# Optimization experiments

Hardware: AMD Instinct MI355X
Metric: run time of the kernel (lower is better)

The kernel has to match this reference:

```python
import jax, jax.numpy as jnp
import numpy as np

B, R, C, OUT, IN = 64, 2048, 32, 32, 16
ROUTING_ITERS = 3


def squash(s, axis=-1):
    s_norm = jnp.linalg.norm(s, axis=axis, keepdims=True)
    scale = s_norm ** 2 / (1.0 + s_norm ** 2)
    return scale * s / (s_norm + 1e-8)


def setup_inputs() -> dict:
    key = jax.random.key(0)
    k1, k2 = jax.random.split(key)
    x = jax.random.normal(k1, (B, R, IN), dtype=jnp.float32)
    W = jax.random.normal(k2, (1, R, C, OUT, IN), dtype=jnp.float32)
    return {"x": x, "W": W}


def reference(x, W):
    # u_hat[b,r,c,o] = sum_i W[r,c,o,i] * x[b,r,i]
    u_hat = jnp.einsum('rcoi,bri->brco', W[0], x)  # [B,R,C,OUT]
    b = jnp.zeros((x.shape[0], R, C), dtype=x.dtype)
    v = None
    for i in range(ROUTING_ITERS):
        c = jax.nn.softmax(b, axis=2)[..., None]       # [B,R,C,1]
        s = jnp.sum(c * u_hat, axis=1)                 # [B,C,OUT]
        v = squash(s)                                  # [B,C,OUT]
        if i < ROUTING_ITERS - 1:
            b = b + jnp.einsum('brco,bco->brc', u_hat, v)
    return v
```

## Files before the change

### kernel.cpp

```cpp
#include <hip/hip_runtime.h>


#define Bn 64
#define Rn 2048
#define Cn 32
#define On 32
#define In 16
#define RCH 16
#define NRC2 (Rn / RCH)
#define NG 2

typedef _Float16 half4v __attribute__((ext_vector_type(4)));
typedef float floatx4 __attribute__((ext_vector_type(4)));

__global__ __launch_bounds__(256)
void wconv(const float* __restrict__ W, _Float16* __restrict__ Wh) {
    const size_t i = ((size_t)blockIdx.x * 256 + threadIdx.x) * 8;
    const float4 a = *(const float4*)(W + i);
    const float4 b = *(const float4*)(W + i + 4);
    union { _Float16 h[8]; uint4 u; } pk;
    pk.h[0] = (_Float16)a.x; pk.h[1] = (_Float16)a.y;
    pk.h[2] = (_Float16)a.z; pk.h[3] = (_Float16)a.w;
    pk.h[4] = (_Float16)b.x; pk.h[5] = (_Float16)b.y;
    pk.h[6] = (_Float16)b.z; pk.h[7] = (_Float16)b.w;
    *(uint4*)(Wh + i) = pk.u;
}

template <int PHASE>
__global__ __launch_bounds__(512, 2)
void upass(const float* __restrict__ x, const _Float16* __restrict__ Wh,
           const float* __restrict__ vroute, float* __restrict__ s_part) {
    const int tid  = threadIdx.x;
    const int w    = tid >> 6;
    const int lane = tid & 63;
    const int q    = lane >> 4;
    const int bl   = lane & 15;

    const int L  = blockIdx.x;
    const int bg = (L >> 3) & 1;
    const int rc = (L & 7) | ((L >> 4) << 3);
    const int b0 = bg * 32;

    __shared__ __attribute__((aligned(16))) _Float16 xs[RCH * 32 * 20];
    __shared__ __attribute__((aligned(16))) float sums[2][2][16][8];

    floatx4 v00[4], v01[4], v10[4], v11[4];
    if constexpr (PHASE > 0) {
        const float* vb0 = vroute + (size_t)(b0 + bl) * 1024 + 4 * q;
        const float* vb1 = vroute + (size_t)(b0 + 16 + bl) * 1024 + 4 * q;
#pragma unroll
        for (int t = 0; t < 4; ++t) {
            const int co = (w * 4 + t) * 32;
            v00[t] = *(const floatx4*)(vb0 + co);
            v01[t] = *(const floatx4*)(vb0 + co + 16);
            v10[t] = *(const floatx4*)(vb1 + co);
            v11[t] = *(const floatx4*)(vb1 + co + 16);
        }
    }

#pragma unroll
    for (int k = 0; k < 4; ++k) {
        const int u  = tid + k * 512;
        const int rr = u >> 7, bb = (u >> 2) & 31, iq = u & 3;
        const float4 xv = *(const float4*)(x + (size_t)(b0 + bb) * (Rn * In) +
                                           (size_t)(rc * RCH + rr) * In + iq * 4);
        union { _Float16 h[4]; uint2 u2; } p;
        p.h[0] = (_Float16)xv.x; p.h[1] = (_Float16)xv.y;
        p.h[2] = (_Float16)xv.z; p.h[3] = (_Float16)xv.w;
        *(uint2*)(xs + (rr * 32 + bb) * 20 + iq * 4) = p.u2;
    }
    __syncthreads();

    floatx4 accS0[8], accS1[8];
#pragma unroll
    for (int m = 0; m < 8; ++m) {
        accS0[m] = (floatx4){0.f, 0.f, 0.f, 0.f};
        accS1[m] = (floatx4){0.f, 0.f, 0.f, 0.f};
    }

    const _Float16* Wp = Wh + ((size_t)(rc * RCH) * 1024 + w * 128 + bl) * 16 + 4 * q;

    half4v a[8];
#pragma unroll
    for (int m = 0; m < 8; ++m) a[m] = *(const half4v*)(Wp + m * 256);
    half4v bf0 = *(const half4v*)(xs + bl * 20 + 4 * q);
    half4v bf1 = *(const half4v*)(xs + (16 + bl) * 20 + 4 * q);

    for (int rr = 0; rr < RCH; ++rr) {
        const int rn = (rr + 1 < RCH) ? rr + 1 : rr;
        const _Float16* Wn = Wp + (size_t)rn * 16384;

        if constexpr (PHASE == 0) {
#pragma unroll
            for (int m = 0; m < 8; ++m) {
                accS0[m] = __builtin_amdgcn_mfma_f32_16x16x16f16(a[m], bf0, accS0[m], 0, 0, 0);
                accS1[m] = __builtin_amdgcn_mfma_f32_16x16x16f16(a[m], bf1, accS1[m], 0, 0, 0);
            }
            const half4v bn0 = *(const half4v*)(xs + (rn * 32 + bl) * 20 + 4 * q);
            const half4v bn1 = *(const half4v*)(xs + (rn * 32 + 16 + bl) * 20 + 4 * q);
#pragma unroll
            for (int m = 0; m < 8; ++m) a[m] = *(const half4v*)(Wn + m * 256);
            bf0 = bn0; bf1 = bn1;
        } else {
            floatx4 D0[8], D1[8];
#pragma unroll
            for (int m = 0; m < 8; ++m) {
                D0[m] = __builtin_amdgcn_mfma_f32_16x16x16f16(
                            a[m], bf0, (floatx4){0.f, 0.f, 0.f, 0.f}, 0, 0, 0);
                D1[m] = __builtin_amdgcn_mfma_f32_16x16x16f16(
                            a[m], bf1, (floatx4){0.f, 0.f, 0.f, 0.f}, 0, 0, 0);
            }

            const half4v bn0 = *(const half4v*)(xs + (rn * 32 + bl) * 20 + 4 * q);
            const half4v bn1 = *(const half4v*)(xs + (rn * 32 + 16 + bl) * 20 + 4 * q);
#pragma unroll
            for (int m = 0; m < 8; ++m) a[m] = *(const half4v*)(Wn + m * 256);
            bf0 = bn0; bf1 = bn1;

            float e0[4], e1[4], se0 = 0.f, se1 = 0.f;
#pragma unroll
            for (int t = 0; t < 4; ++t) {
                float lp0 = D0[2*t].x * v00[t].x + D0[2*t].y * v00[t].y +
                            D0[2*t].z * v00[t].z + D0[2*t].w * v00[t].w +
                            D0[2*t+1].x * v01[t].x + D0[2*t+1].y * v01[t].y +
                            D0[2*t+1].z * v01[t].z + D0[2*t+1].w * v01[t].w;
                float lp1 = D1[2*t].x * v10[t].x + D1[2*t].y * v10[t].y +
                            D1[2*t].z * v10[t].z + D1[2*t].w * v10[t].w +
                            D1[2*t+1].x * v11[t].x + D1[2*t+1].y * v11[t].y +
                            D1[2*t+1].z * v11[t].z + D1[2*t+1].w * v11[t].w;
                lp0 += __shfl_xor(lp0, 16, 64);
                lp0 += __shfl_xor(lp0, 32, 64);
                lp1 += __shfl_xor(lp1, 16, 64);
                lp1 += __shfl_xor(lp1, 32, 64);
                e0[t] = __expf(lp0); se0 += e0[t];
                e1[t] = __expf(lp1); se1 += e1[t];
            }
            if (lane < 32) sums[rr & 1][q][bl][w] = (q == 0) ? se0 : se1;
            asm volatile("s_waitcnt lgkmcnt(0)" ::: "memory");
            __builtin_amdgcn_s_barrier();
            asm volatile("" ::: "memory");
            const floatx4 sa0 = *(const floatx4*)(&sums[rr & 1][0][bl][0]);
            const floatx4 sa1 = *(const floatx4*)(&sums[rr & 1][0][bl][4]);
            const floatx4 sb0 = *(const floatx4*)(&sums[rr & 1][1][bl][0]);
            const floatx4 sb1 = *(const floatx4*)(&sums[rr & 1][1][bl][4]);
            const float tot0 = sa0.x + sa0.y + sa0.z + sa0.w +
                               sa1.x + sa1.y + sa1.z + sa1.w;
            const float tot1 = sb0.x + sb0.y + sb0.z + sb0.w +
                               sb1.x + sb1.y + sb1.z + sb1.w;
            const float winv0 = __builtin_amdgcn_rcpf(tot0);
            const float winv1 = __builtin_amdgcn_rcpf(tot1);
#pragma unroll
            for (int t = 0; t < 4; ++t) {
                const float wt0 = e0[t] * winv0;
                const float wt1 = e1[t] * winv1;
                accS0[2*t]   += wt0 * D0[2*t];
                accS0[2*t+1] += wt0 * D0[2*t+1];
                accS1[2*t]   += wt1 * D1[2*t];
                accS1[2*t+1] += wt1 * D1[2*t+1];
            }
        }
    }

    const size_t sb = (((size_t)rc * 64 + b0 + bl)) * 1024 + w * 128 + 4 * q;
#pragma unroll
    for (int m = 0; m < 8; ++m) {
        *(floatx4*)(s_part + sb + m * 16) = accS0[m];
        *(floatx4*)(s_part + sb + (size_t)16 * 1024 + m * 16) = accS1[m];
    }
}

__global__ __launch_bounds__(256)
void reduce_squash(const float* __restrict__ sp, float scale,
                   float* __restrict__ vout, const float* __restrict__ vprev,
                   float* __restrict__ vsum) {
    const int b = blockIdx.x >> 3, oct = blockIdx.x & 7;
    const int t = threadIdx.x;
    const int kg = t >> 5, ci = t & 31;
    const size_t base = (size_t)b * 1024 + (size_t)oct * 128 + (size_t)ci * 4;

    floatx4 acc0 = (floatx4){0.f, 0.f, 0.f, 0.f};
    floatx4 acc1 = (floatx4){0.f, 0.f, 0.f, 0.f};
#pragma unroll
    for (int k = kg * 16; k < kg * 16 + 16; k += 2) {
        acc0 += *(const floatx4*)(sp + (size_t)k * 65536 + base);
        acc1 += *(const floatx4*)(sp + (size_t)(k + 1) * 65536 + base);
    }
    const floatx4 acc = acc0 + acc1;

    __shared__ __attribute__((aligned(16))) float red[8][128];
    *(floatx4*)(&red[kg][ci * 4]) = acc;
    __syncthreads();

    if (t < 128) {
        float s = 0.f;
#pragma unroll
        for (int g = 0; g < 8; ++g) s += red[g][t];
        s *= scale;
        float n2 = s * s;
        n2 += __shfl_xor(n2, 1, 64);
        n2 += __shfl_xor(n2, 2, 64);
        n2 += __shfl_xor(n2, 4, 64);
        n2 += __shfl_xor(n2, 8, 64);
        n2 += __shfl_xor(n2, 16, 64);
        const float norm = sqrtf(n2);
        const float f = (n2 / (1.f + n2)) / (norm + 1e-8f);
        const float vv = s * f;
        const size_t o = (size_t)b * 1024 + (size_t)oct * 128 + t;
        if (vout) vout[o] = vv;
        if (vsum) vsum[o] = vv + vprev[o];
    }
}

extern "C" void kernel_launch(void* const* d_in, const int* in_sizes, int n_in,
                              void* d_out, int out_size, void* d_ws, size_t ws_size,
                              hipStream_t stream) {
    const float* x = (const float*)d_in[0];
    const float* W = (const float*)d_in[1];
    float* out = (float*)d_out;

    char* ws = (char*)d_ws;
    _Float16* Wh  = (_Float16*)ws;
    float* s_part = (float*)(ws + (size_t)67108864);
    float* v1     = (float*)(ws + (size_t)67108864 + 33554432);
    float* v12    = (float*)(ws + (size_t)67108864 + 33554432 + 262144);

    const int ublocks = NG * NRC2;

    wconv<<<16384, 256, 0, stream>>>(W, Wh);

    upass<0><<<ublocks, 512, 0, stream>>>(x, Wh, nullptr, s_part);
    reduce_squash<<<512, 256, 0, stream>>>(s_part, 1.f / 32.f, v1, nullptr, nullptr);

    upass<1><<<ublocks, 512, 0, stream>>>(x, Wh, v1, s_part);
    reduce_squash<<<512, 256, 0, stream>>>(s_part, 1.f, nullptr, v1, v12);

    upass<2><<<ublocks, 512, 0, stream>>>(x, Wh, v12, s_part);
    reduce_squash<<<512, 256, 0, stream>>>(s_part, 1.f, out, nullptr, nullptr);
}
```

Before: 297.5 us.

## Fuse routing passes into one cooperative kernel with grid syncs

Replaces the six separate upass and reduce_squash launches with a single cooperative kernel of 256 blocks that uses grid-wide syncs between phases. The x tile is converted to fp16 and staged in shared memory once and reused across all three routing iterations instead of being reloaded each pass. This removes kernel launch gaps and repeated x loads, at the cost of grid barrier overhead and a residency requirement that all blocks fit at once.

```diff
diff --git a/kernel.cpp b/kernel.cpp
--- a/kernel.cpp
+++ b/kernel.cpp
@@ -1,4 +1,5 @@
 #include <hip/hip_runtime.h>
+#include <hip/hip_cooperative_groups.h>
 
 
 #define Bn 64
@@ -9,6 +10,8 @@
 #define RCH 16
 #define NRC2 (Rn / RCH)
 #define NG 2
+
+namespace cg = cooperative_groups;
 
 typedef _Float16 half4v __attribute__((ext_vector_type(4)));
 typedef float floatx4 __attribute__((ext_vector_type(4)));
@@ -27,22 +30,10 @@
 }
 
 template <int PHASE>
-__global__ __launch_bounds__(512, 2)
-void upass(const float* __restrict__ x, const _Float16* __restrict__ Wh,
-           const float* __restrict__ vroute, float* __restrict__ s_part) {
-    const int tid  = threadIdx.x;
-    const int w    = tid >> 6;
-    const int lane = tid & 63;
-    const int q    = lane >> 4;
-    const int bl   = lane & 15;
-
-    const int L  = blockIdx.x;
-    const int bg = (L >> 3) & 1;
-    const int rc = (L & 7) | ((L >> 4) << 3);
-    const int b0 = bg * 32;
-
-    __shared__ __attribute__((aligned(16))) _Float16 xs[RCH * 32 * 20];
-    __shared__ __attribute__((aligned(16))) float sums[2][2][16][8];
+__device__ __forceinline__ void upass_dev(
+    const _Float16* __restrict__ Wh, const float* __restrict__ vroute,
+    float* __restrict__ s_part, const _Float16* xs, float (&sums)[2][2][16][8],
+    int w, int lane, int q, int bl, int rc, int b0) {
 
     floatx4 v00[4], v01[4], v10[4], v11[4];
     if constexpr (PHASE > 0) {
@@ -57,19 +48,6 @@
             v11[t] = *(const floatx4*)(vb1 + co + 16);
         }
     }
-
-#pragma unroll
-    for (int k = 0; k < 4; ++k) {
-        const int u  = tid + k * 512;
-        const int rr = u >> 7, bb = (u >> 2) & 31, iq = u & 3;
-        const float4 xv = *(const float4*)(x + (size_t)(b0 + bb) * (Rn * In) +
-                                           (size_t)(rc * RCH + rr) * In + iq * 4);
-        union { _Float16 h[4]; uint2 u2; } p;
-        p.h[0] = (_Float16)xv.x; p.h[1] = (_Float16)xv.y;
-        p.h[2] = (_Float16)xv.z; p.h[3] = (_Float16)xv.w;
-        *(uint2*)(xs + (rr * 32 + bb) * 20 + iq * 4) = p.u2;
-    }
-    __syncthreads();
 
     floatx4 accS0[8], accS1[8];
 #pragma unroll
@@ -169,12 +147,14 @@
     }
 }
 
-__global__ __launch_bounds__(256)
-void reduce_squash(const float* __restrict__ sp, float scale,
-                   float* __restrict__ vout, const float* __restrict__ vprev,
-                   float* __restrict__ vsum) {
-    const int b = blockIdx.x >> 3, oct = blockIdx.x & 7;
-    const int t = threadIdx.x;
+__device__ __forceinline__ void rs_dev(
+    const float* __restrict__ sp, float scale,
+    float* __restrict__ vout, const float* __restrict__ vprev,
+    float* __restrict__ vsum, float (&red)[2][8][128], int tid, int bx) {
+    const int vb = bx * 2 + (tid >> 8);
+    const int half = tid >> 8;
+    const int b = vb >> 3, oct = vb & 7;
+    const int t = tid & 255;
     const int kg = t >> 5, ci = t & 31;
     const size_t base = (size_t)b * 1024 + (size_t)oct * 128 + (size_t)ci * 4;
 
@@ -187,14 +167,13 @@
     }
     const floatx4 acc = acc0 + acc1;
 
-    __shared__ __attribute__((aligned(16))) float red[8][128];
-    *(floatx4*)(&red[kg][ci * 4]) = acc;
+    *(floatx4*)(&red[half][kg][ci * 4]) = acc;
     __syncthreads();
 
     if (t < 128) {
         float s = 0.f;
 #pragma unroll
-        for (int g = 0; g < 8; ++g) s += red[g][t];
+        for (int g = 0; g < 8; ++g) s += red[half][g][t];
         s *= scale;
         float n2 = s * s;
         n2 += __shfl_xor(n2, 1, 64);
@@ -211,6 +190,55 @@
     }
 }
 
+__global__ __launch_bounds__(512, 2)
+void mega(const float* __restrict__ x, const _Float16* __restrict__ Wh,
+          float* __restrict__ s_part, float* __restrict__ v1,
+          float* __restrict__ v12, float* __restrict__ out) {
+    const int tid  = threadIdx.x;
+    const int w    = tid >> 6;
+    const int lane = tid & 63;
+    const int q    = lane >> 4;
+    const int bl   = lane & 15;
+
+    const int L  = blockIdx.x;
+    const int bg = (L >> 3) & 1;
+    const int rc = (L & 7) | ((L >> 4) << 3);
+    const int b0 = bg * 32;
+
+    __shared__ __attribute__((aligned(16))) _Float16 xs[RCH * 32 * 20];
+    __shared__ __attribute__((aligned(16))) float sums[2][2][16][8];
+    __shared__ __attribute__((aligned(16))) float red[2][8][128];
+
+#pragma unroll
+    for (int k = 0; k < 4; ++k) {
+        const int u  = tid + k * 512;
+        const int rr = u >> 7, bb = (u >> 2) & 31, iq = u & 3;
+        const float4 xv = *(const float4*)(x + (size_t)(b0 + bb) * (Rn * In) +
+                                           (size_t)(rc * RCH + rr) * In + iq * 4);
+        union { _Float16 h[4]; uint2 u2; } p;
+        p.h[0] = (_Float16)xv.x; p.h[1] = (_Float16)xv.y;
+        p.h[2] = (_Float16)xv.z; p.h[3] = (_Float16)xv.w;
+        *(uint2*)(xs + (rr * 32 + bb) * 20 + iq * 4) = p.u2;
+    }
+    __syncthreads();
+
+    cg::grid_group gg = cg::this_grid();
+
+    upass_dev<0>(Wh, nullptr, s_part, xs, sums, w, lane, q, bl, rc, b0);
+    __threadfence(); gg.sync();
+    rs_dev(s_part, 1.f / 32.f, v1, nullptr, nullptr, red, tid, L);
+    __threadfence(); gg.sync();
+
+    upass_dev<1>(Wh, v1, s_part, xs, sums, w, lane, q, bl, rc, b0);
+    __threadfence(); gg.sync();
+    rs_dev(s_part, 1.f, nullptr, v1, v12, red, tid, L);
+    __threadfence(); gg.sync();
+
+    upass_dev<2>(Wh, v12, s_part, xs, sums, w, lane, q, bl, rc, b0);
+    __threadfence(); gg.sync();
+    rs_dev(s_part, 1.f, out, nullptr, nullptr, red, tid, L);
+}
+
 extern "C" void kernel_launch(void* const* d_in, const int* in_sizes, int n_in,
                               void* d_out, int out_size, void* d_ws, size_t ws_size,
                               hipStream_t stream) {
@@ -224,16 +252,10 @@
     float* v1     = (float*)(ws + (size_t)67108864 + 33554432);
     float* v12    = (float*)(ws + (size_t)67108864 + 33554432 + 262144);
 
-    const int ublocks = NG * NRC2;
-
     wconv<<<16384, 256, 0, stream>>>(W, Wh);
 
-    upass<0><<<ublocks, 512, 0, stream>>>(x, Wh, nullptr, s_part);
-    reduce_squash<<<512, 256, 0, stream>>>(s_part, 1.f / 32.f, v1, nullptr, nullptr);
-
-    upass<1><<<ublocks, 512, 0, stream>>>(x, Wh, v1, s_part);
-    reduce_squash<<<512, 256, 0, stream>>>(s_part, 1.f, nullptr, v1, v12);
-
-    upass<2><<<ublocks, 512, 0, stream>>>(x, Wh, v12, s_part);
-    reduce_squash<<<512, 256, 0, stream>>>(s_part, 1.f, out, nullptr, nullptr);
-}
+    void* args[6] = {(void*)&x, (void*)&Wh, (void*)&s_part,
+                     (void*)&v1, (void*)&v12, (void*)&out};
+    hipLaunchCooperativeKernel((const void*)mega, dim3(NG * NRC2), dim3(512),
+                               args, 0, stream);
+}
```

Result: slower. 726.1 us (+144.0%).
